# Performance work log

Hardware: AMD Instinct MI355X
Metric: run time of the kernel (lower is better)

The kernel has to match this reference:

```python
import jax, jax.numpy as jnp
import numpy as np

B, S, E, H, D = 4, 2048, 1024, 8, 128
EPS = 1e-5


def _ln(x, g, b):
    m = jnp.mean(x, axis=-1, keepdims=True)
    v = jnp.mean((x - m) ** 2, axis=-1, keepdims=True)
    return (x - m) * jax.lax.rsqrt(v + EPS) * g + b


def _xavier(k, shape, fan_in, fan_out):
    lim = float(np.sqrt(6.0 / (fan_in + fan_out)))
    return jax.random.uniform(k, shape, jnp.float32, -lim, lim)


def setup_inputs() -> dict:
    key = jax.random.key(0)
    ks = jax.random.split(key, 10)
    return {
        "x": jax.random.normal(ks[0], (B, S, E), jnp.float32),
        # embedding_to_z: Linear(E, H*D); stored as [E, H*D] for x @ W
        "W_ez": _xavier(ks[1], (E, H * D), E, H * D),
        "b_ez": jnp.zeros((H * D,), jnp.float32),
        "U_h": _xavier(ks[2], (H, D, D), D, D),
        "U_z": _xavier(ks[3], (H, D, D), D, D),
        "b_u": jnp.zeros((H, D), jnp.float32),
        "out_shaper": _xavier(ks[4], (H, D, D), D, D),
        # shared per-step state LayerNorm
        "lns_g": jnp.ones((D,), jnp.float32),
        "lns_b": jnp.zeros((D,), jnp.float32),
        # per-head FFN: LayerNorm(D) -> Linear(D,D) -> GELU -> Linear(D,E)
        "ff_ln_g": jnp.ones((H, D), jnp.float32),
        "ff_ln_b": jnp.zeros((H, D), jnp.float32),
        "ff_W1": _xavier(ks[5], (H, D, D), D, D),
        "ff_b1": jnp.zeros((H, D), jnp.float32),
        "ff_W2": _xavier(ks[6], (H, D, E), D, E),
        "ff_b2": jnp.zeros((H, E), jnp.float32),
        # layer_attention_weights: Linear(E, 1)
        "w_att": _xavier(ks[7], (E,), E, 1),
        "b_att": jnp.zeros((), jnp.float32),
        # output LayerNorm
        "lno_g": jnp.ones((E,), jnp.float32),
        "lno_b": jnp.zeros((E,), jnp.float32),
    }


def reference(x, W_ez, b_ez, U_h, U_z, b_u, out_shaper, lns_g, lns_b,
              ff_ln_g, ff_ln_b, ff_W1, ff_b1, ff_W2, ff_b2,
              w_att, b_att, lno_g, lno_b):
    b, s, _ = x.shape
    h, d = U_h.shape[0], U_h.shape[1]
    # z tokens: [B,S,H,D]
    z = jnp.tanh((x @ W_ez + b_ez).reshape(b, s, h, d))
    # torch.einsum('bhd,hdd->bhd') takes the DIAGONAL of the second operand
    uh_diag = jnp.einsum('hii->hi', U_h)          # [H,D]
    uz_diag = jnp.einsum('hii->hi', U_z)          # [H,D]
    os_diag = jnp.einsum('hii->hi', out_shaper)   # [H,D]

    def step(h_prev, z_t):
        # h_prev, z_t: [B,H,D]
        u = jax.nn.sigmoid(h_prev * uh_diag + z_t * uz_diag + b_u)
        h_new = u * h_prev + (1.0 - u) * z_t
        h_new = _ln(h_new, lns_g, lns_b)
        return h_new, h_new

    h0 = jnp.zeros((b, h, d), x.dtype)
    _, states = jax.lax.scan(step, h0, jnp.swapaxes(z, 0, 1))  # [S,B,H,D]
    states = jnp.swapaxes(states, 0, 1)                         # [B,S,H,D]

    shaped = states * os_diag                                   # diag einsum
    hln = _ln(shaped, ff_ln_g, ff_ln_b)                         # per-head LN
    h1 = jax.nn.gelu(jnp.einsum('bshd,hde->bshe', hln, ff_W1) + ff_b1,
                     approximate=False)                         # [B,S,H,D]
    ff_out = jnp.einsum('bshd,hde->bshe', h1, ff_W2) + ff_b2    # [B,S,H,E]

    scores = jax.nn.softmax(jnp.einsum('bshe,e->bsh', ff_out, w_att) + b_att,
                            axis=2)                             # over heads
    weighted = jnp.einsum('bshe,bsh->bse', ff_out, scores)      # [B,S,E]
    return _ln(weighted, lno_g, lno_b)
```

## Files before the change

### kernel.cpp

```cpp
#include <hip/hip_runtime.h>
#include <hip/hip_bf16.h>
#include <math.h>

#define BB 4
#define SS 2048
#define EE 1024
#define HH 8
#define DD 128
#define BSR (BB*SS)
#define HD  (HH*DD)
#define LNEPS 1e-5f
#define LOG2E 1.4426950408889634f

#define NCHUNK 16
#define CHS    128
#define NZT    512
#define TPC    64
#define NTICK  (NZT + NCHUNK*TPC)
#define NWORKER 224
#define NSLOT  6
#define SLOTF  (BB*CHS*1024)

#define FSCAN 16
#define FB    32
#define FD    96
#define FE    160
#define FZ    224

typedef __attribute__((ext_vector_type(8))) short bf16x8;
typedef __attribute__((ext_vector_type(4))) float f32x4;

__device__ __forceinline__ ushort f2bf(float f) {
    union { float f; unsigned u; } c{f};
    unsigned r = c.u + 0x7fff + ((c.u >> 16) & 1);
    return (ushort)(r >> 16);
}
__device__ __forceinline__ float bf2f(ushort b) {
    union { unsigned u; float f; } c{(unsigned)b << 16};
    return c.f;
}

typedef __attribute__((address_space(1))) const unsigned int GUI;
typedef __attribute__((address_space(3))) unsigned int LUI;
__device__ __forceinline__ void gl_lds16(const ushort* g, ushort* l) {
    __builtin_amdgcn_global_load_lds((GUI*)g, (LUI*)l, 16, 0, 0);
}

__device__ __forceinline__ float dpp_add(float x, const int ctrl) {
    int y;
    switch (ctrl) {
        case 0x111: y = __builtin_amdgcn_update_dpp(0, __float_as_int(x), 0x111, 0xf, 0xf, true); break;
        case 0x112: y = __builtin_amdgcn_update_dpp(0, __float_as_int(x), 0x112, 0xf, 0xf, true); break;
        case 0x114: y = __builtin_amdgcn_update_dpp(0, __float_as_int(x), 0x114, 0xf, 0xf, true); break;
        case 0x118: y = __builtin_amdgcn_update_dpp(0, __float_as_int(x), 0x118, 0xf, 0xf, true); break;
        case 0x142: y = __builtin_amdgcn_update_dpp(0, __float_as_int(x), 0x142, 0xf, 0xf, true); break;
        default:    y = __builtin_amdgcn_update_dpp(0, __float_as_int(x), 0x143, 0xf, 0xf, true); break;
    }
    return x + __int_as_float(y);
}

__device__ __forceinline__ float wave_sum64(float x) {
    x = dpp_add(x, 0x111);
    x = dpp_add(x, 0x112);
    x = dpp_add(x, 0x114);
    x = dpp_add(x, 0x118);
    x = dpp_add(x, 0x142);
    x = dpp_add(x, 0x143);
    return __int_as_float(__builtin_amdgcn_readlane(__float_as_int(x), 63));
}

__device__ __forceinline__ unsigned flag_peek(unsigned* f) {
    return __hip_atomic_fetch_add(f, 0u, __ATOMIC_RELAXED, __HIP_MEMORY_SCOPE_AGENT);
}
__device__ __forceinline__ void wait_ge(unsigned* f, unsigned tgt) {
    if (threadIdx.x == 0) {
        while (flag_peek(f) < tgt) __builtin_amdgcn_s_sleep(16);
        __builtin_amdgcn_fence(__ATOMIC_ACQUIRE, "agent");
    }
    __syncthreads();
}
__device__ __forceinline__ void wave_wait_ge(unsigned* f, unsigned tgt) {
    unsigned v = 0;
    for (;;) {
        if (threadIdx.x == 0) v = flag_peek(f);
        v = __shfl(v, 0, 64);
        if (v >= tgt) break;
        __builtin_amdgcn_s_sleep(8);
    }
    __builtin_amdgcn_fence(__ATOMIC_ACQUIRE, "agent");
}
__device__ __forceinline__ void done_inc(unsigned* f) {
    __syncthreads();
    if (threadIdx.x == 0) {
        __builtin_amdgcn_fence(__ATOMIC_RELEASE, "agent");
        __hip_atomic_fetch_add(f, 1u, __ATOMIC_RELAXED, __HIP_MEMORY_SCOPE_AGENT);
    }
}
__device__ __forceinline__ unsigned done_inc_ret(unsigned* f, unsigned* sh) {
    __syncthreads();
    if (threadIdx.x == 0) {
        __builtin_amdgcn_fence(__ATOMIC_RELEASE, "agent");
        *sh = __hip_atomic_fetch_add(f, 1u, __ATOMIC_RELAXED, __HIP_MEMORY_SCOPE_AGENT);
    }
    __syncthreads();
    return *sh;
}

__global__ __launch_bounds__(256)
void convx2_k(const float* __restrict__ x,
              ushort* __restrict__ hi, ushort* __restrict__ lo)
{
    const size_t idx = ((size_t)blockIdx.x * 256 + threadIdx.x) * 4;
    const float4 v = *(const float4*)(x + idx);
    ushort4 oh, ol;
    oh.x = f2bf(v.x); ol.x = f2bf(v.x - bf2f(oh.x));
    oh.y = f2bf(v.y); ol.y = f2bf(v.y - bf2f(oh.y));
    oh.z = f2bf(v.z); ol.z = f2bf(v.z - bf2f(oh.z));
    oh.w = f2bf(v.w); ol.w = f2bf(v.w - bf2f(oh.w));
    *(ushort4*)(hi + idx) = oh;
    *(ushort4*)(lo + idx) = ol;
}

__global__ __launch_bounds__(256)
void prepall_k(const float* __restrict__ W_ez,
               ushort* __restrict__ Wth, ushort* __restrict__ Wtl,
               const float* __restrict__ W2, ushort* __restrict__ W2t,
               const float* __restrict__ W1, ushort* __restrict__ W1t,
               const float* __restrict__ w_att, const float* __restrict__ b2,
               const float* __restrict__ b_att,
               const float* __restrict__ Uh, const float* __restrict__ Uz,
               const float* __restrict__ Os,
               float* __restrict__ q, float* __restrict__ c,
               float* __restrict__ uh_d, float* __restrict__ uz_d,
               float* __restrict__ os_d, unsigned* __restrict__ flags)
{
    __shared__ float tile[32][33];
    const int blk = blockIdx.x;
    if (blk == 2434) {
        flags[threadIdx.x] = 0;
        return;
    }
    const int tx = threadIdx.x & 31, ty = threadIdx.x >> 5;
    if (blk < 1024) {
        const int k0 = (blk >> 5) * 32, n0 = (blk & 31) * 32;
        #pragma unroll
        for (int i = 0; i < 4; ++i)
            tile[ty + i*8][tx] = W_ez[(size_t)(k0 + ty + i*8) * 1024 + n0 + tx];
        __syncthreads();
        #pragma unroll
        for (int i = 0; i < 4; ++i) {
            const float v = tile[tx][ty + i*8];
            const ushort h = f2bf(v);
            Wth[(size_t)(n0 + ty + i*8) * 1024 + k0 + tx] = h;
            Wtl[(size_t)(n0 + ty + i*8) * 1024 + k0 + tx] = f2bf(v - bf2f(h));
        }
    } else if (blk < 2048) {
        const int b2i = blk - 1024;
        const int k0 = (b2i >> 5) * 32, n0 = (b2i & 31) * 32;
        #pragma unroll
        for (int i = 0; i < 4; ++i)
            tile[ty + i*8][tx] = W2[(size_t)(k0 + ty + i*8) * 1024 + n0 + tx];
        __syncthreads();
        #pragma unroll
        for (int i = 0; i < 4; ++i)
            W2t[(size_t)(n0 + ty + i*8) * 1024 + k0 + tx] = f2bf(tile[tx][ty + i*8]);
    } else if (blk < 2176) {
        const int idx = blk - 2048;
        const int hh = idx >> 4;
        const int k0 = (idx & 3) * 32, n0 = ((idx >> 2) & 3) * 32;
        const float* Wb = W1 + (size_t)hh * DD * DD;
        ushort*      Wtb = W1t + (size_t)hh * DD * DD;
        #pragma unroll
        for (int i = 0; i < 4; ++i)
            tile[ty + i*8][tx] = Wb[(size_t)(k0 + ty + i*8) * DD + n0 + tx];
        __syncthreads();
        #pragma unroll
        for (int i = 0; i < 4; ++i)
            Wtb[(size_t)(n0 + ty + i*8) * DD + k0 + tx] = f2bf(tile[tx][ty + i*8]);
    } else {
        const int gid  = (blk - 2176) * 256 + threadIdx.x;
        const int wave = gid >> 6, lane = gid & 63;
        if (wave < HD) {
            const float* wp = W2 + (size_t)wave * EE;
            float p = 0.f;
            for (int e = lane; e < EE; e += 64) p = fmaf(wp[e], w_att[e], p);
            #pragma unroll
            for (int off = 32; off > 0; off >>= 1) p += __shfl_xor(p, off, 64);
            if (lane == 0) {
                q[wave] = p;
                const int h = wave >> 7, d = wave & 127;
                uh_d[wave] = Uh[(size_t)h*DD*DD + (size_t)d*DD + d];
                uz_d[wave] = Uz[(size_t)h*DD*DD + (size_t)d*DD + d];
                os_d[wave] = Os[(size_t)h*DD*DD + (size_t)d*DD + d];
            }
        } else if (wave < HD + HH) {
            const int h = wave - HD;
            const float* bp = b2 + (size_t)h * EE;
            float p = 0.f;
            for (int e = lane; e < EE; e += 64) p = fmaf(bp[e], w_att[e], p);
            #pragma unroll
            for (int off = 32; off > 0; off >>= 1) p += __shfl_xor(p, off, 64);
            if (lane == 0) c[h] = p + b_att[0];
        }
    }
}

__global__ __launch_bounds__(256)
void pipeline_k(float* z,
                const ushort* xbh, const ushort* xbl,
                const ushort* __restrict__ Wzh, const ushort* __restrict__ Wzl,
                const float* __restrict__ b_ez,
                const float* __restrict__ uh_d, const float* __restrict__ uz_d,
                const float* __restrict__ b_u,
                const float* __restrict__ lns_g, const float* __restrict__ lns_b,
                ushort* stb,
                const float* __restrict__ os_d,
                const float* __restrict__ ffg, const float* __restrict__ ffb,
                const ushort* __restrict__ W1t, const float* __restrict__ ff_b1,
                const float* __restrict__ qv, const float* __restrict__ cv,
                ushort* __restrict__ h1b, float* __restrict__ logits,
                const ushort* __restrict__ W2t, const float* __restrict__ ff_b2,
                float* __restrict__ wslots,
                const float* __restrict__ lno_g, const float* __restrict__ lno_b,
                float* __restrict__ out,
                unsigned* __restrict__ flags)
{
    __shared__ ushort ldspad[20480];
    if (flags[255] == 0xdeadbeefu)
        ((volatile ushort*)ldspad)[threadIdx.x] = 1;

    if (blockIdx.x < 32) {
        if (threadIdx.x >= 64) return;
        __builtin_amdgcn_s_setprio(3);
        const int bh = blockIdx.x;
        const int b = bh >> 3, h = bh & 7;
        const int l = threadIdx.x;
        const int d0 = 2*l, d1 = d0 + 1;

        const float uhn0 = -uh_d[h*DD+d0] * LOG2E, uhn1 = -uh_d[h*DD+d1] * LOG2E;
        const float uzn0 = -uz_d[h*DD+d0] * LOG2E, uzn1 = -uz_d[h*DD+d1] * LOG2E;
        const float bun0 = -b_u [h*DD+d0] * LOG2E, bun1 = -b_u [h*DD+d1] * LOG2E;
        const float g0  = lns_g[d0], g1 = lns_g[d1];
        const float be0 = lns_b[d0], be1 = lns_b[d1];
        const float A0 = g0 * uhn0, A1 = g1 * uhn1;
        const float bunB0 = fmaf(be0, uhn0, bun0);
        const float bunB1 = fmaf(be1, uhn1, bun1);

        const float* zp = z + ((size_t)b * SS * HH + h) * DD + d0;
        unsigned* op = (unsigned*)(stb + (size_t)b * SS * HD + h * DD) + l;

        wave_wait_ge(&flags[FZ + 0], 32);

        const int CH = 8;
        float2 zc[CH], zn[CH];
        float pb0[CH], pb1[CH];
        #pragma unroll
        for (int i = 0; i < CH; ++i) zc[i] = *(const float2*)(zp + (size_t)i*HD);
        #pragma unroll
        for (int i = 0; i < CH; ++i) {
            pb0[i] = fmaf(zc[i].x, uzn0, bunB0);
            pb1[i] = fmaf(zc[i].y, uzn1, bunB1);
        }

        float r_c, wp0, wp1, W0, W1, dv0, dv1;

#define PACK_STORE(HP0, HP1, OFF) do {                                       \
            const unsigned pu0 = __float_as_uint(HP0) + 0x8000u;             \
            const unsigned pu1 = __float_as_uint(HP1) + 0x8000u;             \
            op[(size_t)(OFF) * (HD/2)] =                                     \
                __builtin_amdgcn_perm(pu1, pu0, 0x07060302u);                \
        } while (0)

#define SCAN_STEP(ZX, ZY, PB0v, PB1v, ZNX, ZNY, OFF) do {                    \
            const float t0 = fmaf(r_c, W0, (PB0v));                          \
            const float t1 = fmaf(r_c, W1, (PB1v));                          \
            const float e0 = __builtin_amdgcn_exp2f(t0);                     \
            const float e1 = __builtin_amdgcn_exp2f(t1);                     \
            const float u0 = __builtin_amdgcn_rcpf(1.f + e0);                \
            const float u1 = __builtin_amdgcn_rcpf(1.f + e1);                \
            const float hn0 = fmaf(u0, dv0, (ZX));                           \
            const float hn1 = fmaf(u1, dv1, (ZY));                           \
            const float s1 = wave_sum64(hn0 + hn1);                          \
            const float s2 = wave_sum64(fmaf(hn0, hn0, hn1*hn1));            \
            const float m   = s1 * (1.f/128.f);                              \
            const float var = fmaf(s2, 1.f/128.f, -m*m);                     \
            r_c = __builtin_amdgcn_rsqf(var + LNEPS);                        \
            wp0 = hn0 - m; wp1 = hn1 - m;                                    \
            W0 = wp0 * A0; W1 = wp1 * A1;                                    \
            const float hp0 = fmaf(wp0, r_c * g0, be0);                      \
            const float hp1 = fmaf(wp1, r_c * g1, be1);                      \
            PACK_STORE(hp0, hp1, OFF);                                       \
            dv0 = hp0 - (ZNX); dv1 = hp1 - (ZNY);                            \
        } while (0)

        {
            const float z0 = zc[0].x, z1 = zc[0].y;
            const float t0 = fmaf(z0, uzn0, bun0);
            const float t1 = fmaf(z1, uzn1, bun1);
            const float e0 = __builtin_amdgcn_exp2f(t0);
            const float e1 = __builtin_amdgcn_exp2f(t1);
            const float u0 = __builtin_amdgcn_rcpf(1.f + e0);
            const float u1 = __builtin_amdgcn_rcpf(1.f + e1);
            const float hn0 = fmaf(u0, -z0, z0);
            const float hn1 = fmaf(u1, -z1, z1);
            const float s1 = wave_sum64(hn0 + hn1);
            const float s2 = wave_sum64(fmaf(hn0, hn0, hn1*hn1));
            const float m   = s1 * (1.f/128.f);
            const float var = fmaf(s2, 1.f/128.f, -m*m);
            r_c = __builtin_amdgcn_rsqf(var + LNEPS);
            wp0 = hn0 - m; wp1 = hn1 - m;
            W0 = wp0 * A0; W1 = wp1 * A1;
            const float hp0 = fmaf(wp0, r_c * g0, be0);
            const float hp1 = fmaf(wp1, r_c * g1, be1);
            PACK_STORE(hp0, hp1, 0);
            dv0 = hp0 - zc[1].x; dv1 = hp1 - zc[1].y;
        }

        #pragma unroll
        for (int i = 0; i < CH; ++i)
            zn[i] = *(const float2*)(zp + (size_t)(CH+i)*HD);
        #pragma unroll
        for (int i = 1; i < CH; ++i) {
            const float znx = (i+1 < CH) ? zc[i+1].x : zn[0].x;
            const float zny = (i+1 < CH) ? zc[i+1].y : zn[0].y;
            SCAN_STEP(zc[i].x, zc[i].y, pb0[i], pb1[i], znx, zny, i);
        }
        #pragma unroll
        for (int i = 0; i < CH; ++i) {
            zc[i] = zn[i];
            pb0[i] = fmaf(zn[i].x, uzn0, bunB0);
            pb1[i] = fmaf(zn[i].y, uzn1, bunB1);
        }

        for (int s0 = CH; s0 < SS; s0 += CH) {
            if (s0 + CH < SS) {
                if (((s0 + CH) & (CHS-1)) == 0)
                    wave_wait_ge(&flags[FZ + ((s0 + CH) >> 7)], 32);
                #pragma unroll
                for (int i = 0; i < CH; ++i)
                    zn[i] = *(const float2*)(zp + (size_t)(s0+CH+i)*HD);
            } else {
                #pragma unroll
                for (int i = 0; i < CH; ++i) zn[i] = make_float2(0.f, 0.f);
            }
            #pragma unroll
            for (int i = 0; i < CH; ++i) {
                const float znx = (i+1 < CH) ? zc[i+1].x : zn[0].x;
                const float zny = (i+1 < CH) ? zc[i+1].y : zn[0].y;
                SCAN_STEP(zc[i].x, zc[i].y, pb0[i], pb1[i], znx, zny, s0 + i);
            }
            #pragma unroll
            for (int i = 0; i < CH; ++i) {
                zc[i] = zn[i];
                pb0[i] = fmaf(zn[i].x, uzn0, bunB0);
                pb1[i] = fmaf(zn[i].y, uzn1, bunB1);
            }
            if ((s0 & (CHS-1)) == CHS - CH) {
                if (threadIdx.x == 0) {
                    __builtin_amdgcn_fence(__ATOMIC_RELEASE, "agent");
                    __hip_atomic_fetch_add(&flags[FSCAN + (s0 >> 7)], 1u,
                                           __ATOMIC_RELAXED, __HIP_MEMORY_SCOPE_AGENT);
                }
            }
        }
#undef SCAN_STEP
#undef PACK_STORE
        return;
    }

    __shared__ ushort ApS[4*128*32];
    __shared__ ushort Bsm[128*32];
    __shared__ float  sLDS[128][8];
    __shared__ float  lpart[128][2];
    __shared__ unsigned s_tk, s_old;
    const int tid = threadIdx.x;
    const int lane = tid & 63, w = tid >> 6;
    const int wr = w >> 1, wc = w & 1;
    const int lr = lane >> 2;
    const int lc = (lane & 3) ^ (lr & 3);
    const int quad = lane >> 4;
    const int fr   = lane & 15;
    const int fchk = (quad ^ (lane & 3)) * 8;

    for (;;) {
        __syncthreads();
        if (tid == 0) s_tk = __hip_atomic_fetch_add(&flags[0], 1u,
                               __ATOMIC_RELAXED, __HIP_MEMORY_SCOPE_AGENT);
        __syncthreads();
        const unsigned tk = s_tk;
        if (tk >= NTICK) return;

        if (tk < NZT) {
            const int zc = (int)(tk >> 5), zb = (int)((tk >> 3) & 3), zy = (int)(tk & 7);
            const int row0 = zb*SS + zc*CHS, col0 = zy*128;
            ushort* AH = ApS;
            ushort* AL = ApS + 4096;
            ushort* BH = ApS + 8192;
            ushort* BL = ApS + 12288;
            const size_t aoff0 = (size_t)(row0 +      w*16 + lr) * 1024 + lc*8;
            const size_t aoff1 = (size_t)(row0 + 64 + w*16 + lr) * 1024 + lc*8;
            const size_t boff0 = (size_t)(col0 +      w*16 + lr) * 1024 + lc*8;
            const size_t boff1 = (size_t)(col0 + 64 + w*16 + lr) * 1024 + lc*8;
            ushort* AH0 = AH + (     w*16) * 32;  ushort* AH1 = AH + (64 + w*16) * 32;
            ushort* AL0 = AL + (     w*16) * 32;  ushort* AL1 = AL + (64 + w*16) * 32;
            ushort* BH0 = BH + (     w*16) * 32;  ushort* BH1 = BH + (64 + w*16) * 32;
            ushort* BL0 = BL + (     w*16) * 32;  ushort* BL1 = BL + (64 + w*16) * 32;

            f32x4 acc[4][4];
            #pragma unroll
            for (int i = 0; i < 4; ++i)
                #pragma unroll
                for (int j = 0; j < 4; ++j) acc[i][j] = (f32x4){0.f,0.f,0.f,0.f};

            for (int k0 = 0; k0 < 1024; k0 += 32) {
                __syncthreads();
                gl_lds16(xbh + aoff0 + k0, AH0);
                gl_lds16(xbh + aoff1 + k0, AH1);
                gl_lds16(Wzh + boff0 + k0, BH0);
                gl_lds16(Wzh + boff1 + k0, BH1);
                gl_lds16(xbl + aoff0 + k0, AL0);
                gl_lds16(xbl + aoff1 + k0, AL1);
                gl_lds16(Wzl + boff0 + k0, BL0);
                gl_lds16(Wzl + boff1 + k0, BL1);
                __syncthreads();

                bf16x8 afh[4], afl[4], bfh[4], bfl[4];
                #pragma unroll
                for (int i = 0; i < 4; ++i) {
                    const int ra = (wr*64 + i*16 + fr) * 32 + fchk;
                    afh[i] = *(const bf16x8*)(AH + ra);
                    afl[i] = *(const bf16x8*)(AL + ra);
                    const int rb = (wc*64 + i*16 + fr) * 32 + fchk;
                    bfh[i] = *(const bf16x8*)(BH + rb);
                    bfl[i] = *(const bf16x8*)(BL + rb);
                }
                #pragma unroll
                for (int i = 0; i < 4; ++i)
                    #pragma unroll
                    for (int j = 0; j < 4; ++j) {
                        acc[i][j] = __builtin_amdgcn_mfma_f32_16x16x32_bf16(
                            afh[i], bfl[j], acc[i][j], 0, 0, 0);
                        acc[i][j] = __builtin_amdgcn_mfma_f32_16x16x32_bf16(
                            afl[i], bfh[j], acc[i][j], 0, 0, 0);
                        acc[i][j] = __builtin_amdgcn_mfma_f32_16x16x32_bf16(
                            afh[i], bfh[j], acc[i][j], 0, 0, 0);
                    }
            }

            float colv[4];
            #pragma unroll
            for (int tj = 0; tj < 4; ++tj)
                colv[tj] = b_ez[col0 + wc*64 + tj*16 + fr];
            #pragma unroll
            for (int ti = 0; ti < 4; ++ti)
                #pragma unroll
                for (int i = 0; i < 4; ++i) {
                    const int row = row0 + wr*64 + ti*16 + quad*4 + i;
                    #pragma unroll
                    for (int tj = 0; tj < 4; ++tj) {
                        const int col = col0 + wc*64 + tj*16 + fr;
                        z[(size_t)row*1024 + col] = tanhf(acc[ti][tj][i] + colv[tj]);
                    }
                }
            done_inc(&flags[FZ + zc]);
            continue;
        }

        const unsigned t2 = tk - NZT;
        const int c = (int)(t2 / TPC);
        const int r = (int)(t2 % TPC);

        if (r < 32) {
            wait_ge(&flags[FSCAN + c], 32);
            const int bb = r >> 3, hh = r & 7;
            const int row0 = bb*SS + c*CHS;

            {
                const int l = lane;
                const int d0 = 2*l, d1 = d0 + 1;
                const float osd0 = os_d[hh*DD + d0], osd1 = os_d[hh*DD + d1];
                const float fg0 = ffg[hh*DD + d0], fg1 = ffg[hh*DD + d1];
                const float fb0 = ffb[hh*DD + d0], fb1 = ffb[hh*DD + d1];
                const unsigned* st_u = (const unsigned*)stb;
                const int p  = l >> 4;
                const int j  = (l >> 2) & 3;
                unsigned* ApU = (unsigned*)ApS;
                for (int it = 0; it < 32; ++it) {
                    const int rloc = it*4 + w;
                    const unsigned v = st_u[(size_t)(row0 + rloc)*512 + hh*64 + l];
                    const float x0 = bf2f((ushort)(v & 0xffff)) * osd0;
                    const float x1 = bf2f((ushort)(v >> 16))    * osd1;
                    float s1 = x0 + x1;
                    float s2 = fmaf(x0, x0, x1*x1);
                    #pragma unroll
                    for (int off = 32; off > 0; off >>= 1) {
                        s1 += __shfl_xor(s1, off, 64);
                        s2 += __shfl_xor(s2, off, 64);
                    }
                    const float m   = s1 * (1.f/128.f);
                    const float var = fmaf(s2, 1.f/128.f, -m*m);
                    const float rr  = rsqrtf(var + LNEPS);
                    const float o0 = fmaf((x0 - m)*rr, fg0, fb0);
                    const float o1 = fmaf((x1 - m)*rr, fg1, fb1);
                    const unsigned pv = (unsigned)f2bf(o0) | ((unsigned)f2bf(o1) << 16);
                    const int js = j ^ (rloc & 3);
                    ApU[p*2048 + rloc*16 + js*4 + (l & 3)] = pv;
                }
            }
            __syncthreads();

            const ushort* Bg0 = W1t + (size_t)hh*DD*DD + (     w*16 + lr) * DD + lc*8;
            const ushort* Bg1 = W1t + (size_t)hh*DD*DD + (64 + w*16 + lr) * DD + lc*8;
            ushort* Bl0 = Bsm + (     w*16) * 32;
            ushort* Bl1 = Bsm + (64 + w*16) * 32;

            f32x4 acc[4][4];
            #pragma unroll
            for (int i = 0; i < 4; ++i)
                #pragma unroll
                for (int j2 = 0; j2 < 4; ++j2) acc[i][j2] = (f32x4){0.f,0.f,0.f,0.f};

            for (int k0 = 0; k0 < 128; k0 += 32) {
                __syncthreads();
                gl_lds16(Bg0 + k0, Bl0);
                gl_lds16(Bg1 + k0, Bl1);
                __syncthreads();

                const ushort* Ap = ApS + (k0 >> 5) * 4096;
                bf16x8 af[4], bf[4];
                #pragma unroll
                for (int i = 0; i < 4; ++i) {
                    af[i] = *(const bf16x8*)(Ap + (wr*64 + i*16 + fr)*32 + fchk);
                    bf[i] = *(const bf16x8*)(Bsm + (wc*64 + i*16 + fr)*32 + fchk);
                }
                #pragma unroll
                for (int i = 0; i < 4; ++i)
                    #pragma unroll
                    for (int j2 = 0; j2 < 4; ++j2)
                        acc[i][j2] = __builtin_amdgcn_mfma_f32_16x16x32_bf16(
                            af[i], bf[j2], acc[i][j2], 0, 0, 0);
            }

            float colv[4], qh[4];
            #pragma unroll
            for (int tj = 0; tj < 4; ++tj) {
                const int col = wc*64 + tj*16 + fr;
                colv[tj] = ff_b1[hh*DD + col];
                qh[tj]   = qv[hh*DD + col];
            }
            #pragma unroll
            for (int ti = 0; ti < 4; ++ti)
                #pragma unroll
                for (int i = 0; i < 4; ++i) {
                    const int row = row0 + wr*64 + ti*16 + quad*4 + i;
                    float p = 0.f;
                    #pragma unroll
                    for (int tj = 0; tj < 4; ++tj) {
                        const int col = wc*64 + tj*16 + fr;
                        float v = acc[ti][tj][i] + colv[tj];
                        v = 0.5f * v * (1.f + erff(v * 0.70710678118654752f));
                        h1b[(size_t)row*1024 + hh*DD + col] = f2bf(v);
                        p = fmaf(v, qh[tj], p);
                    }
                    p = dpp_add(p, 0x111);
                    p = dpp_add(p, 0x112);
                    p = dpp_add(p, 0x114);
                    p = dpp_add(p, 0x118);
                    if (fr == 15)
                        lpart[wr*64 + ti*16 + quad*4 + i][wc] = p;
                }
            __syncthreads();
            if (tid < 128)
                logits[(size_t)(row0 + tid)*HH + hh] = lpart[tid][0] + lpart[tid][1] + cv[hh];
            done_inc(&flags[FB + c*4 + bb]);
        } else {
            const int sub = r - 32;
            const int bb = sub >> 3, cb = sub & 7;
            wait_ge(&flags[FB + c*4 + bb], 8);
            if (c >= NSLOT) wait_ge(&flags[FE + (c-NSLOT)*4 + bb], 1);
            const int row0 = bb*SS + c*CHS, col0 = cb*128;
            float* wslot = wslots + (size_t)(c % NSLOT) * SLOTF;

            if (tid < 128) {
                const float4 l03 = *(const float4*)(logits + (size_t)(row0 + tid)*8);
                const float4 l47 = *(const float4*)(logits + (size_t)(row0 + tid)*8 + 4);
                float lv[8] = {l03.x,l03.y,l03.z,l03.w,l47.x,l47.y,l47.z,l47.w};
                float mx = -1e30f;
                #pragma unroll
                for (int i = 0; i < 8; ++i) mx = fmaxf(mx, lv[i]);
                float den = 0.f;
                #pragma unroll
                for (int i = 0; i < 8; ++i) den += __expf(lv[i] - mx);
                const float rden = 1.f / den;
                #pragma unroll
                for (int i = 0; i < 8; ++i) sLDS[tid][i] = __expf(lv[i] - mx) * rden;
            }
            __syncthreads();

            const ushort* Bg0 = W2t + (size_t)(col0 +      w*16 + lr) * 1024 + lc*8;
            const ushort* Bg1 = W2t + (size_t)(col0 + 64 + w*16 + lr) * 1024 + lc*8;
            ushort* Bl0 = Bsm + (     w*16) * 32;
            ushort* Bl1 = Bsm + (64 + w*16) * 32;
            const int rl0 = w*16 + lr, rl1 = 64 + w*16 + lr;

            f32x4 acc[4][4];
            #pragma unroll
            for (int i = 0; i < 4; ++i)
                #pragma unroll
                for (int j2 = 0; j2 < 4; ++j2) acc[i][j2] = (f32x4){0.f,0.f,0.f,0.f};

            for (int k0 = 0; k0 < 1024; k0 += 32) {
                __syncthreads();
                {
                    const int kk = k0 + lc*8;
                    const int hidx = kk >> 7;
                    bf16x8 a0 = *(const bf16x8*)(h1b + (size_t)(row0 + rl0)*1024 + kk);
                    bf16x8 a1 = *(const bf16x8*)(h1b + (size_t)(row0 + rl1)*1024 + kk);
                    const float sc0 = sLDS[rl0][hidx];
                    const float sc1 = sLDS[rl1][hidx];
                    bf16x8 w0, w1;
                    #pragma unroll
                    for (int e = 0; e < 8; ++e) {
                        w0[e] = (short)f2bf(bf2f((ushort)a0[e]) * sc0);
                        w1[e] = (short)f2bf(bf2f((ushort)a1[e]) * sc1);
                    }
                    *(bf16x8*)(ApS + (     w*16)*32 + lane*8) = w0;
                    *(bf16x8*)(ApS + (64 + w*16)*32 + lane*8) = w1;
                }
                gl_lds16(Bg0 + k0, Bl0);
                gl_lds16(Bg1 + k0, Bl1);
                __syncthreads();

                bf16x8 af[4], bf[4];
                #pragma unroll
                for (int i = 0; i < 4; ++i) {
                    af[i] = *(const bf16x8*)(ApS + (wr*64 + i*16 + fr)*32 + fchk);
                    bf[i] = *(const bf16x8*)(Bsm + (wc*64 + i*16 + fr)*32 + fchk);
                }
                #pragma unroll
                for (int i = 0; i < 4; ++i)
                    #pragma unroll
                    for (int j2 = 0; j2 < 4; ++j2)
                        acc[i][j2] = __builtin_amdgcn_mfma_f32_16x16x32_bf16(
                            af[i], bf[j2], acc[i][j2], 0, 0, 0);
            }

            float b2v[4][HH];
            #pragma unroll
            for (int tj = 0; tj < 4; ++tj) {
                const int col = col0 + wc*64 + tj*16 + fr;
                #pragma unroll
                for (int h = 0; h < HH; ++h) b2v[tj][h] = ff_b2[(size_t)h*EE + col];
            }
            #pragma unroll
            for (int ti = 0; ti < 4; ++ti)
                #pragma unroll
                for (int i = 0; i < 4; ++i) {
                    const int lrow = wr*64 + ti*16 + quad*4 + i;
                    float sc[HH];
                    #pragma unroll
                    for (int h = 0; h < HH; ++h) sc[h] = sLDS[lrow][h];
                    #pragma unroll
                    for (int tj = 0; tj < 4; ++tj) {
                        const int col = col0 + wc*64 + tj*16 + fr;
                        float bbv = 0.f;
                        #pragma unroll
                        for (int h = 0; h < HH; ++h) bbv = fmaf(sc[h], b2v[tj][h], bbv);
                        wslot[(size_t)(bb*128 + lrow)*1024 + col] = acc[ti][tj][i] + bbv;
                    }
                }

            const unsigned old = done_inc_ret(&flags[FD + c*4 + bb], &s_old);
            if (old == 7) {
                if (tid == 0) __builtin_amdgcn_fence(__ATOMIC_ACQUIRE, "agent");
                __syncthreads();
                const float* wsE = wslots + (size_t)(c % NSLOT) * SLOTF
                                 + (size_t)bb * 128 * 1024;
                float4 gvq[4], bvq[4];
                #pragma unroll
                for (int q4 = 0; q4 < 4; ++q4) {
                    gvq[q4] = *(const float4*)(lno_g + lane*4 + q4*256);
                    bvq[q4] = *(const float4*)(lno_b + lane*4 + q4*256);
                }
                for (int it = 0; it < 32; ++it) {
                    const int rloc = it*4 + w;
                    const float* wp = wsE + (size_t)rloc*1024;
                    float4 vq[4];
                    float s1 = 0.f, s2 = 0.f;
                    #pragma unroll
                    for (int q4 = 0; q4 < 4; ++q4) {
                        vq[q4] = *(const float4*)(wp + lane*4 + q4*256);
                        s1 += vq[q4].x + vq[q4].y + vq[q4].z + vq[q4].w;
                        s2 += vq[q4].x*vq[q4].x + vq[q4].y*vq[q4].y
                            + vq[q4].z*vq[q4].z + vq[q4].w*vq[q4].w;
                    }
                    #pragma unroll
                    for (int off = 32; off > 0; off >>= 1) {
                        s1 += __shfl_xor(s1, off, 64);
                        s2 += __shfl_xor(s2, off, 64);
                    }
                    const float m   = s1 * (1.f/1024.f);
                    const float var = fmaf(s2, 1.f/1024.f, -m*m);
                    const float rr  = rsqrtf(var + LNEPS);
                    float* op = out + (size_t)(row0 + rloc)*1024;
                    #pragma unroll
                    for (int q4 = 0; q4 < 4; ++q4) {
                        float4 o;
                        o.x = fmaf((vq[q4].x - m)*rr, gvq[q4].x, bvq[q4].x);
                        o.y = fmaf((vq[q4].y - m)*rr, gvq[q4].y, bvq[q4].y);
                        o.z = fmaf((vq[q4].z - m)*rr, gvq[q4].z, bvq[q4].z);
                        o.w = fmaf((vq[q4].w - m)*rr, gvq[q4].w, bvq[q4].w);
                        *(float4*)(op + lane*4 + q4*256) = o;
                    }
                }
                done_inc(&flags[FE + c*4 + bb]);
            }
        }
    }
}

extern "C" void kernel_launch(void* const* d_in, const int* in_sizes, int n_in,
                              void* d_out, int out_size, void* d_ws, size_t ws_size,
                              hipStream_t stream)
{
    const float* x       = (const float*)d_in[0];
    const float* W_ez    = (const float*)d_in[1];
    const float* b_ez    = (const float*)d_in[2];
    const float* U_h     = (const float*)d_in[3];
    const float* U_z     = (const float*)d_in[4];
    const float* b_u     = (const float*)d_in[5];
    const float* outsh   = (const float*)d_in[6];
    const float* lns_g   = (const float*)d_in[7];
    const float* lns_b   = (const float*)d_in[8];
    const float* ff_ln_g = (const float*)d_in[9];
    const float* ff_ln_b = (const float*)d_in[10];
    const float* ff_W1   = (const float*)d_in[11];
    const float* ff_b1   = (const float*)d_in[12];
    const float* ff_W2   = (const float*)d_in[13];
    const float* ff_b2   = (const float*)d_in[14];
    const float* w_att   = (const float*)d_in[15];
    const float* b_att   = (const float*)d_in[16];
    const float* lno_g   = (const float*)d_in[17];
    const float* lno_b   = (const float*)d_in[18];
    float* out = (float*)d_out;

    float* ws = (float*)d_ws;
    const size_t NBIG = (size_t)BSR * HD;
    float* bufA = ws;
    float* bufB = ws + NBIG;
    float* bufC = ws + 2*NBIG;
    float* ext  = ws + 3*NBIG;
    ushort* W2t   = (ushort*)ext;
    ushort* W1t   = (ushort*)(ext + 512*1024);
    float* logits = ext + 512*1024 + 64*1024;
    float* qv     = logits + BSR*HH;
    float* cv     = qv + HD;
    float* uh_d   = cv + 8;
    float* uz_d   = uh_d + HD;
    float* os_d   = uz_d + HD;
    unsigned* flags = (unsigned*)(os_d + HD);
    ushort* xb_hi = (ushort*)bufB;
    ushort* xb_lo = (ushort*)bufB + NBIG;
    ushort* stb   = (ushort*)bufB;
    ushort* h1b     = (ushort*)bufC;
    float*  wslots  = bufC + 4*1024*1024;
    ushort* WezT_hi = (ushort*)(bufC + 7*1024*1024);
    ushort* WezT_lo = WezT_hi + 1024*1024;

    convx2_k<<<(BSR*EE/4)/256, 256, 0, stream>>>(x, xb_hi, xb_lo);
    prepall_k<<<2435, 256, 0, stream>>>(W_ez, WezT_hi, WezT_lo,
                                        ff_W2, W2t, ff_W1, W1t,
                                        w_att, ff_b2, b_att,
                                        U_h, U_z, outsh,
                                        qv, cv, uh_d, uz_d, os_d, flags);
    pipeline_k<<<32 + NWORKER, 256, 0, stream>>>(
        bufA, xb_hi, xb_lo, WezT_hi, WezT_lo, b_ez,
        uh_d, uz_d, b_u, lns_g, lns_b, stb,
        os_d, ff_ln_g, ff_ln_b,
        W1t, ff_b1, qv, cv, h1b, logits,
        W2t, ff_b2, wslots,
        lno_g, lno_b, out, flags);
}
```

Baseline: 615.8 us.

## Fold input conversion and weight prep into persistent pipeline as flagged tasks

Removes the separate x-to-bf16-split and weight-prep kernels and turns their work into ticketed tasks inside the persistent pipeline kernel. Input conversion now runs per sequence chunk, and new flags let each z-GEMM tile start once its chunk and the transposed W_ez are ready, so the recurrent scan can begin before all of x is converted. The later stages now wait on flags for the transposed W1 and W2 and the attention constants. The scan's z prefetch depth also doubles from 8 to 16. The cost is extra flag polling, more tickets, and more LDS per block.

```diff
diff --git a/kernel.cpp b/kernel.cpp
--- a/kernel.cpp
+++ b/kernel.cpp
@@ -14,10 +14,17 @@
 
 #define NCHUNK 16
 #define CHS    128
-#define NZT    512
+#define NQC    4
+#define CONV0B 4
+#define WEZB   12
+#define Z0B    44
+#define W2TB   76
+#define W1TB   108
+#define CONV1B 112
+#define Z1B    232
+#define STAGEB 712
 #define TPC    64
-#define NTICK  (NZT + NCHUNK*TPC)
-#define NWORKER 224
+#define NTICK  (STAGEB + NCHUNK*TPC)
 #define NSLOT  6
 #define SLOTF  (BB*CHS*1024)
 
@@ -26,6 +33,11 @@
 #define FD    96
 #define FE    160
 #define FZ    224
+#define FCONV 240
+#define FQC   256
+#define FWEZ  257
+#define FW2T  258
+#define FW1T  259
 
 typedef __attribute__((ext_vector_type(8))) short bf16x8;
 typedef __attribute__((ext_vector_type(4))) float f32x4;
@@ -107,126 +119,39 @@
 }
 
 __global__ __launch_bounds__(256)
-void convx2_k(const float* __restrict__ x,
-              ushort* __restrict__ hi, ushort* __restrict__ lo)
+void zerof_k(unsigned* __restrict__ flags)
 {
-    const size_t idx = ((size_t)blockIdx.x * 256 + threadIdx.x) * 4;
-    const float4 v = *(const float4*)(x + idx);
-    ushort4 oh, ol;
-    oh.x = f2bf(v.x); ol.x = f2bf(v.x - bf2f(oh.x));
-    oh.y = f2bf(v.y); ol.y = f2bf(v.y - bf2f(oh.y));
-    oh.z = f2bf(v.z); ol.z = f2bf(v.z - bf2f(oh.z));
-    oh.w = f2bf(v.w); ol.w = f2bf(v.w - bf2f(oh.w));
-    *(ushort4*)(hi + idx) = oh;
-    *(ushort4*)(lo + idx) = ol;
+    flags[threadIdx.x] = 0;
+    flags[256 + threadIdx.x] = 0;
 }
 
 __global__ __launch_bounds__(256)
-void prepall_k(const float* __restrict__ W_ez,
-               ushort* __restrict__ Wth, ushort* __restrict__ Wtl,
-               const float* __restrict__ W2, ushort* __restrict__ W2t,
-               const float* __restrict__ W1, ushort* __restrict__ W1t,
-               const float* __restrict__ w_att, const float* __restrict__ b2,
-               const float* __restrict__ b_att,
-               const float* __restrict__ Uh, const float* __restrict__ Uz,
-               const float* __restrict__ Os,
-               float* __restrict__ q, float* __restrict__ c,
-               float* __restrict__ uh_d, float* __restrict__ uz_d,
-               float* __restrict__ os_d, unsigned* __restrict__ flags)
-{
-    __shared__ float tile[32][33];
-    const int blk = blockIdx.x;
-    if (blk == 2434) {
-        flags[threadIdx.x] = 0;
-        return;
-    }
-    const int tx = threadIdx.x & 31, ty = threadIdx.x >> 5;
-    if (blk < 1024) {
-        const int k0 = (blk >> 5) * 32, n0 = (blk & 31) * 32;
-        #pragma unroll
-        for (int i = 0; i < 4; ++i)
-            tile[ty + i*8][tx] = W_ez[(size_t)(k0 + ty + i*8) * 1024 + n0 + tx];
-        __syncthreads();
-        #pragma unroll
-        for (int i = 0; i < 4; ++i) {
-            const float v = tile[tx][ty + i*8];
-            const ushort h = f2bf(v);
-            Wth[(size_t)(n0 + ty + i*8) * 1024 + k0 + tx] = h;
-            Wtl[(size_t)(n0 + ty + i*8) * 1024 + k0 + tx] = f2bf(v - bf2f(h));
-        }
-    } else if (blk < 2048) {
-        const int b2i = blk - 1024;
-        const int k0 = (b2i >> 5) * 32, n0 = (b2i & 31) * 32;
-        #pragma unroll
-        for (int i = 0; i < 4; ++i)
-            tile[ty + i*8][tx] = W2[(size_t)(k0 + ty + i*8) * 1024 + n0 + tx];
-        __syncthreads();
-        #pragma unroll
-        for (int i = 0; i < 4; ++i)
-            W2t[(size_t)(n0 + ty + i*8) * 1024 + k0 + tx] = f2bf(tile[tx][ty + i*8]);
-    } else if (blk < 2176) {
-        const int idx = blk - 2048;
-        const int hh = idx >> 4;
-        const int k0 = (idx & 3) * 32, n0 = ((idx >> 2) & 3) * 32;
-        const float* Wb = W1 + (size_t)hh * DD * DD;
-        ushort*      Wtb = W1t + (size_t)hh * DD * DD;
-        #pragma unroll
-        for (int i = 0; i < 4; ++i)
-            tile[ty + i*8][tx] = Wb[(size_t)(k0 + ty + i*8) * DD + n0 + tx];
-        __syncthreads();
-        #pragma unroll
-        for (int i = 0; i < 4; ++i)
-            Wtb[(size_t)(n0 + ty + i*8) * DD + k0 + tx] = f2bf(tile[tx][ty + i*8]);
-    } else {
-        const int gid  = (blk - 2176) * 256 + threadIdx.x;
-        const int wave = gid >> 6, lane = gid & 63;
-        if (wave < HD) {
-            const float* wp = W2 + (size_t)wave * EE;
-            float p = 0.f;
-            for (int e = lane; e < EE; e += 64) p = fmaf(wp[e], w_att[e], p);
-            #pragma unroll
-            for (int off = 32; off > 0; off >>= 1) p += __shfl_xor(p, off, 64);
-            if (lane == 0) {
-                q[wave] = p;
-                const int h = wave >> 7, d = wave & 127;
-                uh_d[wave] = Uh[(size_t)h*DD*DD + (size_t)d*DD + d];
-                uz_d[wave] = Uz[(size_t)h*DD*DD + (size_t)d*DD + d];
-                os_d[wave] = Os[(size_t)h*DD*DD + (size_t)d*DD + d];
-            }
-        } else if (wave < HD + HH) {
-            const int h = wave - HD;
-            const float* bp = b2 + (size_t)h * EE;
-            float p = 0.f;
-            for (int e = lane; e < EE; e += 64) p = fmaf(bp[e], w_att[e], p);
-            #pragma unroll
-            for (int off = 32; off > 0; off >>= 1) p += __shfl_xor(p, off, 64);
-            if (lane == 0) c[h] = p + b_att[0];
-        }
-    }
-}
-
-__global__ __launch_bounds__(256)
-void pipeline_k(float* z,
-                const ushort* xbh, const ushort* xbl,
-                const ushort* __restrict__ Wzh, const ushort* __restrict__ Wzl,
-                const float* __restrict__ b_ez,
-                const float* __restrict__ uh_d, const float* __restrict__ uz_d,
+void pipeline_k(float* __restrict__ z,
+                const float* __restrict__ xg,
+                const float* __restrict__ Wez, const float* __restrict__ b_ez,
+                const float* __restrict__ W2, const float* __restrict__ W1,
+                const float* __restrict__ w_att, const float* __restrict__ b_att,
+                const float* __restrict__ Uh, const float* __restrict__ Uz,
+                const float* __restrict__ Os,
                 const float* __restrict__ b_u,
                 const float* __restrict__ lns_g, const float* __restrict__ lns_b,
                 ushort* stb,
-                const float* __restrict__ os_d,
+                ushort* xbh, ushort* __restrict__ xbl,
+                ushort* __restrict__ Wzh, ushort* __restrict__ Wzl,
                 const float* __restrict__ ffg, const float* __restrict__ ffb,
-                const ushort* __restrict__ W1t, const float* __restrict__ ff_b1,
-                const float* __restrict__ qv, const float* __restrict__ cv,
+                ushort* __restrict__ W1t, const float* __restrict__ ff_b1,
+                float* __restrict__ qv, float* __restrict__ cv,
+                float* __restrict__ uh_d, float* __restrict__ uz_d,
+                float* __restrict__ os_d,
                 ushort* __restrict__ h1b, float* __restrict__ logits,
-                const ushort* __restrict__ W2t, const float* __restrict__ ff_b2,
+                ushort* __restrict__ W2t, const float* __restrict__ ff_b2,
                 float* __restrict__ wslots,
                 const float* __restrict__ lno_g, const float* __restrict__ lno_b,
                 float* __restrict__ out,
                 unsigned* __restrict__ flags)
 {
     __shared__ ushort ldspad[20480];
-    if (flags[255] == 0xdeadbeefu)
+    if (flags[300] == 0xdeadbeefu)
         ((volatile ushort*)ldspad)[threadIdx.x] = 1;
 
     if (blockIdx.x < 32) {
@@ -236,6 +161,8 @@
         const int b = bh >> 3, h = bh & 7;
         const int l = threadIdx.x;
         const int d0 = 2*l, d1 = d0 + 1;
+
+        wave_wait_ge(&flags[FQC], NQC);
 
         const float uhn0 = -uh_d[h*DD+d0] * LOG2E, uhn1 = -uh_d[h*DD+d1] * LOG2E;
         const float uzn0 = -uz_d[h*DD+d0] * LOG2E, uzn1 = -uz_d[h*DD+d1] * LOG2E;
@@ -251,7 +178,7 @@
 
         wave_wait_ge(&flags[FZ + 0], 32);
 
-        const int CH = 8;
+        const int CH = 16;
         float2 zc[CH], zn[CH];
         float pb0[CH], pb1[CH];
         #pragma unroll
@@ -262,7 +189,7 @@
             pb1[i] = fmaf(zc[i].y, uzn1, bunB1);
         }
 
-        float r_c, wp0, wp1, W0, W1, dv0, dv1;
+        float r_c, wp0, wp1, W0, W1r, dv0, dv1;
 
 #define PACK_STORE(HP0, HP1, OFF) do {                                       \
             const unsigned pu0 = __float_as_uint(HP0) + 0x8000u;             \
@@ -273,7 +200,7 @@
 
 #define SCAN_STEP(ZX, ZY, PB0v, PB1v, ZNX, ZNY, OFF) do {                    \
             const float t0 = fmaf(r_c, W0, (PB0v));                          \
-            const float t1 = fmaf(r_c, W1, (PB1v));                          \
+            const float t1 = fmaf(r_c, W1r, (PB1v));                         \
             const float e0 = __builtin_amdgcn_exp2f(t0);                     \
             const float e1 = __builtin_amdgcn_exp2f(t1);                     \
             const float u0 = __builtin_amdgcn_rcpf(1.f + e0);                \
@@ -286,7 +213,7 @@
             const float var = fmaf(s2, 1.f/128.f, -m*m);                     \
             r_c = __builtin_amdgcn_rsqf(var + LNEPS);                        \
             wp0 = hn0 - m; wp1 = hn1 - m;                                    \
-            W0 = wp0 * A0; W1 = wp1 * A1;                                    \
+            W0 = wp0 * A0; W1r = wp1 * A1;                                   \
             const float hp0 = fmaf(wp0, r_c * g0, be0);                      \
             const float hp1 = fmaf(wp1, r_c * g1, be1);                      \
             PACK_STORE(hp0, hp1, OFF);                                       \
@@ -309,7 +236,7 @@
             const float var = fmaf(s2, 1.f/128.f, -m*m);
             r_c = __builtin_amdgcn_rsqf(var + LNEPS);
             wp0 = hn0 - m; wp1 = hn1 - m;
-            W0 = wp0 * A0; W1 = wp1 * A1;
+            W0 = wp0 * A0; W1r = wp1 * A1;
             const float hp0 = fmaf(wp0, r_c * g0, be0);
             const float hp1 = fmaf(wp1, r_c * g1, be1);
             PACK_STORE(hp0, hp1, 0);
@@ -372,6 +299,7 @@
     __shared__ ushort Bsm[128*32];
     __shared__ float  sLDS[128][8];
     __shared__ float  lpart[128][2];
+    __shared__ float  ttile[32][33];
     __shared__ unsigned s_tk, s_old;
     const int tid = threadIdx.x;
     const int lane = tid & 63, w = tid >> 6;
@@ -381,6 +309,7 @@
     const int quad = lane >> 4;
     const int fr   = lane & 15;
     const int fchk = (quad ^ (lane & 3)) * 8;
+    const int tx = tid & 31, ty = tid >> 5;
 
     for (;;) {
         __syncthreads();
@@ -390,9 +319,88 @@
         const unsigned tk = s_tk;
         if (tk >= NTICK) return;
 
-        if (tk < NZT) {
-            const int zc = (int)(tk >> 5), zb = (int)((tk >> 3) & 3), zy = (int)(tk & 7);
-            const int row0 = zb*SS + zc*CHS, col0 = zy*128;
+        if (tk < CONV0B) {
+            const int base = (int)tk * 258;
+            for (int it = 0; it < 65; ++it) {
+                const int wv = base + it*4 + w;
+                if (wv >= base + 258 || wv >= HD + HH) continue;
+                if (wv < HD) {
+                    const float* wp = W2 + (size_t)wv * EE;
+                    float pp = 0.f;
+                    for (int e = lane; e < EE; e += 64) pp = fmaf(wp[e], w_att[e], pp);
+                    #pragma unroll
+                    for (int off = 32; off > 0; off >>= 1) pp += __shfl_xor(pp, off, 64);
+                    if (lane == 0) {
+                        qv[wv] = pp;
+                        const int hq = wv >> 7, dq = wv & 127;
+                        uh_d[wv] = Uh[(size_t)hq*DD*DD + (size_t)dq*DD + dq];
+                        uz_d[wv] = Uz[(size_t)hq*DD*DD + (size_t)dq*DD + dq];
+                        os_d[wv] = Os[(size_t)hq*DD*DD + (size_t)dq*DD + dq];
+                    }
+                } else {
+                    const int hq = wv - HD;
+                    const float* bp = ff_b2 + (size_t)hq * EE;
+                    float pp = 0.f;
+                    for (int e = lane; e < EE; e += 64) pp = fmaf(bp[e], w_att[e], pp);
+                    #pragma unroll
+                    for (int off = 32; off > 0; off >>= 1) pp += __shfl_xor(pp, off, 64);
+                    if (lane == 0) cv[hq] = pp + b_att[0];
+                }
+            }
+            done_inc(&flags[FQC]);
+            continue;
+        }
+
+        if (tk < WEZB || (tk >= CONV1B && tk < Z1B)) {
+            int c, i;
+            if (tk < WEZB) { c = 0; i = (int)tk - CONV0B; }
+            else { const int t = (int)tk - CONV1B; c = 1 + (t >> 3); i = t & 7; }
+            const int r0 = (i >> 1)*SS + c*CHS + (i & 1)*64;
+            for (int it = 0; it < 64; ++it) {
+                const size_t off = (size_t)(r0 + it)*1024 + tid*4;
+                const float4 v = *(const float4*)(xg + off);
+                ushort4 oh, ol;
+                oh.x = f2bf(v.x); ol.x = f2bf(v.x - bf2f(oh.x));
+                oh.y = f2bf(v.y); ol.y = f2bf(v.y - bf2f(oh.y));
+                oh.z = f2bf(v.z); ol.z = f2bf(v.z - bf2f(oh.z));
+                oh.w = f2bf(v.w); ol.w = f2bf(v.w - bf2f(oh.w));
+                *(ushort4*)(xbh + off) = oh;
+                *(ushort4*)(xbl + off) = ol;
+            }
+            done_inc(&flags[FCONV + c]);
+            continue;
+        }
+
+        if (tk < Z0B) {
+            const int p = (int)tk - WEZB;
+            for (int i5 = 0; i5 < 32; ++i5) {
+                const int t2i = p*32 + i5;
+                const int k0 = (t2i >> 5) * 32, n0 = (t2i & 31) * 32;
+                __syncthreads();
+                #pragma unroll
+                for (int ii = 0; ii < 4; ++ii)
+                    ttile[ty + ii*8][tx] = Wez[(size_t)(k0 + ty + ii*8)*1024 + n0 + tx];
+                __syncthreads();
+                #pragma unroll
+                for (int ii = 0; ii < 4; ++ii) {
+                    const float v = ttile[tx][ty + ii*8];
+                    const ushort hv = f2bf(v);
+                    Wzh[(size_t)(n0 + ty + ii*8)*1024 + k0 + tx] = hv;
+                    Wzl[(size_t)(n0 + ty + ii*8)*1024 + k0 + tx] = f2bf(v - bf2f(hv));
+                }
+            }
+            done_inc(&flags[FWEZ]);
+            continue;
+        }
+
+        if (tk < W2TB || (tk >= Z1B && tk < STAGEB)) {
+            int c, idx;
+            if (tk < W2TB) { c = 0; idx = (int)tk - Z0B; }
+            else { const int t = (int)tk - Z1B; c = 1 + (t >> 5); idx = t & 31; }
+            wait_ge(&flags[FCONV + c], 8);
+            wait_ge(&flags[FWEZ], 32);
+            const int zb = idx >> 3, zy = idx & 7;
+            const int row0 = zb*SS + c*CHS, col0 = zy*128;
             ushort* AH = ApS;
             ushort* AL = ApS + 4096;
             ushort* BH = ApS + 8192;
@@ -462,16 +470,59 @@
                         z[(size_t)row*1024 + col] = tanhf(acc[ti][tj][i] + colv[tj]);
                     }
                 }
-            done_inc(&flags[FZ + zc]);
+            done_inc(&flags[FZ + c]);
             continue;
         }
 
-        const unsigned t2 = tk - NZT;
+        if (tk < W1TB) {
+            const int p = (int)tk - W2TB;
+            for (int i5 = 0; i5 < 32; ++i5) {
+                const int t2i = p*32 + i5;
+                const int k0 = (t2i >> 5) * 32, n0 = (t2i & 31) * 32;
+                __syncthreads();
+                #pragma unroll
+                for (int ii = 0; ii < 4; ++ii)
+                    ttile[ty + ii*8][tx] = W2[(size_t)(k0 + ty + ii*8)*1024 + n0 + tx];
+                __syncthreads();
+                #pragma unroll
+                for (int ii = 0; ii < 4; ++ii)
+                    W2t[(size_t)(n0 + ty + ii*8)*1024 + k0 + tx] =
+                        f2bf(ttile[tx][ty + ii*8]);
+            }
+            done_inc(&flags[FW2T]);
+            continue;
+        }
+
+        if (tk < CONV1B) {
+            const int p = (int)tk - W1TB;
+            for (int i5 = 0; i5 < 32; ++i5) {
+                const int idx = p*32 + i5;
+                const int hh = idx >> 4;
+                const int k0 = (idx & 3)*32, n0 = ((idx >> 2) & 3)*32;
+                const float* Wb = W1 + (size_t)hh * DD * DD;
+                ushort*     Wtb = W1t + (size_t)hh * DD * DD;
+                __syncthreads();
+                #pragma unroll
+                for (int ii = 0; ii < 4; ++ii)
+                    ttile[ty + ii*8][tx] = Wb[(size_t)(k0 + ty + ii*8)*DD + n0 + tx];
+                __syncthreads();
+                #pragma unroll
+                for (int ii = 0; ii < 4; ++ii)
+                    Wtb[(size_t)(n0 + ty + ii*8)*DD + k0 + tx] =
+                        f2bf(ttile[tx][ty + ii*8]);
+            }
+            done_inc(&flags[FW1T]);
+            continue;
+        }
+
+        const unsigned t2 = tk - STAGEB;
         const int c = (int)(t2 / TPC);
         const int r = (int)(t2 % TPC);
 
         if (r < 32) {
             wait_ge(&flags[FSCAN + c], 32);
+            wait_ge(&flags[FW1T], 4);
+            wait_ge(&flags[FQC], NQC);
             const int bb = r >> 3, hh = r & 7;
             const int row0 = bb*SS + c*CHS;
 
@@ -577,6 +628,7 @@
             const int sub = r - 32;
             const int bb = sub >> 3, cb = sub & 7;
             wait_ge(&flags[FB + c*4 + bb], 8);
+            wait_ge(&flags[FW2T], 32);
             if (c >= NSLOT) wait_ge(&flags[FE + (c-NSLOT)*4 + bb], 1);
             const int row0 = bb*SS + c*CHS, col0 = cb*128;
             float* wslot = wslots + (size_t)(c % NSLOT) * SLOTF;
@@ -767,17 +819,12 @@
     ushort* WezT_hi = (ushort*)(bufC + 7*1024*1024);
     ushort* WezT_lo = WezT_hi + 1024*1024;
 
-    convx2_k<<<(BSR*EE/4)/256, 256, 0, stream>>>(x, xb_hi, xb_lo);
-    prepall_k<<<2435, 256, 0, stream>>>(W_ez, WezT_hi, WezT_lo,
-                                        ff_W2, W2t, ff_W1, W1t,
-                                        w_att, ff_b2, b_att,
-                                        U_h, U_z, outsh,
-                                        qv, cv, uh_d, uz_d, os_d, flags);
-    pipeline_k<<<32 + NWORKER, 256, 0, stream>>>(
-        bufA, xb_hi, xb_lo, WezT_hi, WezT_lo, b_ez,
-        uh_d, uz_d, b_u, lns_g, lns_b, stb,
-        os_d, ff_ln_g, ff_ln_b,
-        W1t, ff_b1, qv, cv, h1b, logits,
-        W2t, ff_b2, wslots,
+    zerof_k<<<1, 256, 0, stream>>>(flags);
+    pipeline_k<<<256, 256, 0, stream>>>(
+        bufA, x, W_ez, b_ez, ff_W2, ff_W1, w_att, b_att,
+        U_h, U_z, outsh, b_u, lns_g, lns_b,
+        stb, xb_hi, xb_lo, WezT_hi, WezT_lo,
+        ff_ln_g, ff_ln_b, W1t, ff_b1, qv, cv, uh_d, uz_d, os_d,
+        h1b, logits, W2t, ff_b2, wslots,
         lno_g, lno_b, out, flags);
 }
```

Measured after the change: 932.8 us. +51.5%, slower.
